# Kernel optimization log

Measured on AMD Instinct MI355X. Metric: run time of the kernel, lower is better.

Reference implementation:

```python
import jax, jax.numpy as jnp
import numpy as np
import math

NUM_HEADS = 12
EXPAND = 3  # head_expand -> DLA hidden = 36
BN_EPS = 1e-5


def conv2d(x, w, groups=1):
    # x: [B,C,H,W], w: [O, I/groups, kh, kw], stride 1, SAME padding (Conv2dSame)
    return jax.lax.conv_general_dilated(
        x, w, window_strides=(1, 1), padding='SAME',
        dimension_numbers=('NCHW', 'OIHW', 'NCHW'), feature_group_count=groups)


def batchnorm(x, gamma, beta):
    # training-mode BatchNorm2d: batch statistics over (B, H, W) per channel
    mean = jnp.mean(x, axis=(0, 2, 3), keepdims=True)
    var = jnp.var(x, axis=(0, 2, 3), keepdims=True)
    xn = (x - mean) * jax.lax.rsqrt(var + BN_EPS)
    return xn * gamma[None, :, None, None] + beta[None, :, None, None]


def setup_inputs() -> dict:
    key = jax.random.key(0)
    ks = jax.random.split(key, 8)
    B, N, C = 32, 196, 768
    H = NUM_HEADS
    hidden = H * EXPAND  # 36
    s = 0.02
    inp = {
        'x': jax.random.normal(ks[0], (B, N, C), dtype=jnp.float32),
        'w_qkv': jax.random.normal(ks[1], (3 * C, C), dtype=jnp.float32) * s,
        'w_exp': jax.random.normal(ks[2], (hidden, H, 1, 1), dtype=jnp.float32) * 0.1,
        'bn1_g': jnp.ones((hidden,), jnp.float32), 'bn1_b': jnp.zeros((hidden,), jnp.float32),
        'w_dw': jax.random.normal(ks[3], (hidden, 1, 3, 3), dtype=jnp.float32) * 0.1,
        'bn2_g': jnp.ones((hidden,), jnp.float32), 'bn2_b': jnp.zeros((hidden,), jnp.float32),
        'w_pro': jax.random.normal(ks[4], (H, hidden, 1, 1), dtype=jnp.float32) * 0.1,
        'bn3_g': jnp.ones((H,), jnp.float32), 'bn3_b': jnp.zeros((H,), jnp.float32),
        'abn_g': jnp.ones((H,), jnp.float32), 'abn_b': jnp.zeros((H,), jnp.float32),
        'w_proj': jax.random.normal(ks[5], (C, C), dtype=jnp.float32) * s,
        'b_proj': jnp.zeros((C,), jnp.float32),
    }
    return inp


def reference(x, w_qkv, w_exp, bn1_g, bn1_b, w_dw, bn2_g, bn2_b,
              w_pro, bn3_g, bn3_b, abn_g, abn_b, w_proj, b_proj):
    B, N, C = x.shape
    H = NUM_HEADS
    d = C // H
    hidden = H * EXPAND
    scale = d ** (-0.5)
    rs = math.sqrt(scale)

    # qkv: [B,N,3C] -> [3,B,H,N,d]
    qkv = (x @ w_qkv.T).reshape(B, N, 3, H, d).transpose(2, 0, 3, 1, 4)
    q = qkv[0] * rs
    k = qkv[1] * rs
    v = qkv[2]

    attn = jax.nn.softmax(jnp.einsum('bhnd,bhmd->bhnm', q, k), axis=-1)

    # DLA (conv_exapnd): 1x1 expand -> BN -> ReLU6 -> 3x3 depthwise -> BN -> ReLU6 -> 1x1 project -> BN
    y = conv2d(attn, w_exp)                       # [B, 36, N, N]
    y = jnp.clip(batchnorm(y, bn1_g, bn1_b), 0.0, 6.0)
    y = conv2d(y, w_dw, groups=hidden)            # depthwise 3x3
    y = jnp.clip(batchnorm(y, bn2_g, bn2_b), 0.0, 6.0)
    y = conv2d(y, w_pro)                          # [B, 12, N, N]
    y = batchnorm(y, bn3_g, bn3_b)
    attn_r = batchnorm(y, abn_g, abn_b)           # adapt_bn

    out = jnp.einsum('bhnm,bhmd->bhnd', attn_r, v)  # [B,H,N,d]
    out = out.transpose(0, 2, 1, 3).reshape(B, N, C)
    out = out @ w_proj.T + b_proj
    return out, attn_r
```

## Files before the change

### kernel.cpp

```cpp
#include <hip/hip_runtime.h>
#include <hip/hip_bf16.h>
#include <hip/hip_fp16.h>
#include <math.h>

constexpr int Bz  = 32;
constexpr int Nn  = 196;
constexpr int Cc  = 768;
constexpr int Hh  = 12;
constexpr int Dd  = 64;
constexpr int NN2 = Nn * Nn;
constexpr int QSZ = Bz * Nn * Cc;
constexpr int ATT = Bz * Hh * NN2;
constexpr int SAMP = Bz * NN2;
constexpr float RS = 0.35355339059327373f;
constexpr int CHUNK = 7056;
constexpr int NCACHE = 6076;
constexpr int RA_CAP = 4181;
constexpr int RB_CAP = 1365;

typedef short bf16x8 __attribute__((ext_vector_type(8)));
typedef float f32x4  __attribute__((ext_vector_type(4)));

__device__ inline ushort f2b(float f) {
  __hip_bfloat16 h = __float2bfloat16(f);
  return *reinterpret_cast<ushort*>(&h);
}
__device__ inline float b2f(ushort u) {
  union { float f; unsigned i; } x; x.i = ((unsigned)u) << 16; return x.f;
}
__device__ inline ushort f2h_(float f) {
  __half h = __float2half(f);
  return *reinterpret_cast<ushort*>(&h);
}
__device__ inline float h2f_(ushort u) {
  __half h = *reinterpret_cast<__half*>(&u);
  return __half2float(h);
}
__device__ inline const ushort* y2chunk_r(int blk, const ushort* rA, const ushort* rB,
                                          const ushort* rC) {
  if (blk < RA_CAP) return rA + (size_t)blk*CHUNK;
  if (blk < RA_CAP + RB_CAP) return rB + (size_t)(blk - RA_CAP)*CHUNK;
  return rC + (size_t)(blk - RA_CAP - RB_CAP)*CHUNK;
}
__device__ inline ushort* y2chunk_w(int blk, ushort* rA, ushort* rB, ushort* rC) {
  if (blk < RA_CAP) return rA + (size_t)blk*CHUNK;
  if (blk < RA_CAP + RB_CAP) return rB + (size_t)(blk - RA_CAP)*CHUNK;
  return rC + (size_t)(blk - RA_CAP - RB_CAP)*CHUNK;
}

__global__ __launch_bounds__(256) void k_cast(const float* __restrict__ in,
                                              ushort* __restrict__ outp) {
  const int j = blockIdx.x*256 + threadIdx.x;
  float4 a = ((const float4*)in)[2*j];
  float4 b = ((const float4*)in)[2*j+1];
  ushort o[8] = { f2b(a.x), f2b(a.y), f2b(a.z), f2b(a.w),
                  f2b(b.x), f2b(b.y), f2b(b.z), f2b(b.w) };
  ((uint4*)outp)[j] = *(const uint4*)o;
}

template<int EPI>
__global__ __launch_bounds__(256) void k_mfma_gemm(const ushort* __restrict__ A,
                                                   const ushort* __restrict__ B,
                                                   const float* __restrict__ bias,
                                                   void* __restrict__ o0,
                                                   void* __restrict__ o1,
                                                   void* __restrict__ o2) {
  __shared__ ushort As[128*72];
  __shared__ ushort Bs[128*72];
  const int t = threadIdx.x;
  const int m0 = blockIdx.y*128, n0 = blockIdx.x*128;
  const int w = t>>6, lane = t&63;
  const int wr = w>>1, wc = w&1;
  const int lrow = lane&15, lkb = lane>>4;
  f32x4 acc[4][4] = {};
  const int srow = t>>1, skoff = (t&1)*32;
  const ushort* aP = A + (size_t)(m0+srow)*768 + skoff;
  const ushort* bP = B + (size_t)(n0+srow)*768 + skoff;
  ushort* aw = &As[srow*72 + skoff];
  ushort* bw = &Bs[srow*72 + skoff];
  for (int k0 = 0; k0 < 768; k0 += 64) {
    uint4 a0 = *(const uint4*)(aP+k0),    a1 = *(const uint4*)(aP+k0+8);
    uint4 a2 = *(const uint4*)(aP+k0+16), a3 = *(const uint4*)(aP+k0+24);
    uint4 b0 = *(const uint4*)(bP+k0),    b1 = *(const uint4*)(bP+k0+8);
    uint4 b2 = *(const uint4*)(bP+k0+16), b3 = *(const uint4*)(bP+k0+24);
    __syncthreads();
    *(uint4*)(aw)    = a0; *(uint4*)(aw+8)  = a1;
    *(uint4*)(aw+16) = a2; *(uint4*)(aw+24) = a3;
    *(uint4*)(bw)    = b0; *(uint4*)(bw+8)  = b1;
    *(uint4*)(bw+16) = b2; *(uint4*)(bw+24) = b3;
    __syncthreads();
#pragma unroll
    for (int kk = 0; kk < 2; kk++) {
      bf16x8 af[4], bfr[4];
#pragma unroll
      for (int m = 0; m < 4; m++)
        af[m] = *(const bf16x8*)&As[(wr*64+m*16+lrow)*72 + kk*32 + lkb*8];
#pragma unroll
      for (int n = 0; n < 4; n++)
        bfr[n] = *(const bf16x8*)&Bs[(wc*64+n*16+lrow)*72 + kk*32 + lkb*8];
#pragma unroll
      for (int m = 0; m < 4; m++)
#pragma unroll
        for (int n = 0; n < 4; n++)
          acc[m][n] = __builtin_amdgcn_mfma_f32_16x16x32_bf16(af[m], bfr[n], acc[m][n], 0, 0, 0);
    }
  }
  const int r4 = lane>>4;
#pragma unroll
  for (int m = 0; m < 4; m++) {
#pragma unroll
    for (int r = 0; r < 4; r++) {
      const int grow = m0 + wr*64 + m*16 + r4*4 + r;
      if (EPI == 0) {
        ushort* q = (ushort*)o0; ushort* k = (ushort*)o1; ushort* v = (ushort*)o2;
        const int b = grow/196, nn = grow - b*196;
#pragma unroll
        for (int n = 0; n < 4; n++) {
          const int gcol = n0 + wc*64 + n*16 + lrow;
          const int three = gcol/768, rem = gcol - three*768;
          const int h = rem>>6, dd = rem&63;
          float val = acc[m][n][r] * (three < 2 ? RS : 1.0f);
          ushort* base = (three == 0) ? q : (three == 1) ? k : v;
          base[((size_t)(b*12+h)*196 + nn)*64 + dd] = f2b(val);
        }
      } else {
        float* outp = (float*)o0;
#pragma unroll
        for (int n = 0; n < 4; n++) {
          const int gcol = n0 + wc*64 + n*16 + lrow;
          outp[(size_t)grow*768 + gcol] = acc[m][n][r] + bias[gcol];
        }
      }
    }
  }
}

__global__ __launch_bounds__(256) void k_qks(const ushort* __restrict__ qb,
                                             const ushort* __restrict__ kb,
                                             float* __restrict__ attn) {
  __shared__ ushort K_lds[208*68];
  const int t = threadIdx.x;
  const int bh = blockIdx.x;
  const ushort* kp = kb + (size_t)bh*Nn*Dd;
  const ushort* qp = qb + (size_t)bh*Nn*Dd;
  for (int i = t; i < 1568; i += 256) {
    int row = i >> 3, ko = (i & 7)*8;
    *(uint4*)&K_lds[row*68 + ko] = *(const uint4*)(kp + (size_t)row*64 + ko);
  }
  for (int i = t; i < 408; i += 256)
    ((unsigned*)&K_lds[196*68])[i] = 0u;
  __syncthreads();
  const int w = t >> 6, lane = t & 63;
  const int slot = blockIdx.y*4 + w;
  if (slot >= 13) return;
  const int lrow = lane & 15, lk = lane >> 4;
  int qrow = slot*16 + lrow; if (qrow > 195) qrow = 195;
  bf16x8 aq0 = *(const bf16x8*)(qp + (size_t)qrow*64 + lk*8);
  bf16x8 aq1 = *(const bf16x8*)(qp + (size_t)qrow*64 + 32 + lk*8);
  f32x4 acc[13];
#pragma unroll
  for (int nt = 0; nt < 13; nt++) {
    f32x4 a = {};
    bf16x8 b0 = *(const bf16x8*)&K_lds[(nt*16 + lrow)*68 + lk*8];
    a = __builtin_amdgcn_mfma_f32_16x16x32_bf16(aq0, b0, a, 0, 0, 0);
    bf16x8 b1 = *(const bf16x8*)&K_lds[(nt*16 + lrow)*68 + 32 + lk*8];
    acc[nt] = __builtin_amdgcn_mfma_f32_16x16x32_bf16(aq1, b1, a, 0, 0, 0);
  }
  const bool tailok = (lrow < 4);
  float inv[4];
#pragma unroll
  for (int r = 0; r < 4; r++) {
    float mx = -1e30f;
#pragma unroll
    for (int nt = 0; nt < 12; nt++) mx = fmaxf(mx, acc[nt][r]);
    if (tailok) mx = fmaxf(mx, acc[12][r]);
    mx = fmaxf(mx, __shfl_xor(mx, 1, 64));
    mx = fmaxf(mx, __shfl_xor(mx, 2, 64));
    mx = fmaxf(mx, __shfl_xor(mx, 4, 64));
    mx = fmaxf(mx, __shfl_xor(mx, 8, 64));
    float s = 0.0f;
#pragma unroll
    for (int nt = 0; nt < 13; nt++) {
      bool valid = (nt < 12) || tailok;
      float e = valid ? __expf(acc[nt][r] - mx) : 0.0f;
      acc[nt][r] = e;
      s += e;
    }
    s += __shfl_xor(s, 1, 64);
    s += __shfl_xor(s, 2, 64);
    s += __shfl_xor(s, 4, 64);
    s += __shfl_xor(s, 8, 64);
    inv[r] = 1.0f / s;
  }
  const int rowb = slot*16 + lk*4;
#pragma unroll
  for (int r = 0; r < 4; r++) {
    const int row = rowb + r;
    if (row < 196) {
      float* op = attn + ((size_t)bh*196 + row)*196;
#pragma unroll
      for (int nt = 0; nt < 13; nt++) {
        int col = nt*16 + lrow;
        if (col < 196) op[col] = acc[nt][r]*inv[r];
      }
    }
  }
}

__global__ __launch_bounds__(256) void k_gram(const float* __restrict__ attn,
                                              float* __restrict__ part) {
  __shared__ float red2[4*78];
  const int t = threadIdx.x;
  float m[78] = {};
  const int stride = gridDim.x * 256;
  for (int s = blockIdx.x*256 + t; s < SAMP; s += stride) {
    int b = s / NN2, p = s - b*NN2;
    float a[12];
#pragma unroll
    for (int h = 0; h < 12; h++) a[h] = attn[((size_t)(b*12+h))*NN2 + p];
    int idx = 0;
#pragma unroll
    for (int h = 0; h < 12; h++)
#pragma unroll
      for (int h2 = h; h2 < 12; h2++, idx++) m[idx] = fmaf(a[h], a[h2], m[idx]);
  }
#pragma unroll
  for (int i = 0; i < 78; i++) {
#pragma unroll
    for (int off = 32; off; off >>= 1) m[i] += __shfl_xor(m[i], off, 64);
  }
  const int w = t >> 6;
  if ((t & 63) == 0) {
#pragma unroll
    for (int i = 0; i < 78; i++) red2[w*78 + i] = m[i];
  }
  __syncthreads();
  if (t < 78)
    part[(size_t)blockIdx.x*78 + t] = red2[t] + red2[78+t] + red2[156+t] + red2[234+t];
}

__global__ __launch_bounds__(256) void k_reduce(const float* __restrict__ part, int nb,
                                               int stride, double* __restrict__ dsum) {
  __shared__ double sh[256];
  const int c = blockIdx.x;
  const int t = threadIdx.x;
  double s = 0.0;
  for (int i = t; i < nb; i += 256) s += (double)part[(size_t)i*stride + c];
  sh[t] = s;
  __syncthreads();
  for (int o = 128; o; o >>= 1) {
    if (t < o) sh[t] += sh[t + o];
    __syncthreads();
  }
  if (t == 0) dsum[c] = sh[0];
}

__global__ void k_bn1gram(const double* __restrict__ dsum,
                          const float* __restrict__ w_exp,
                          const float* __restrict__ g, const float* __restrict__ beta,
                          float* __restrict__ stats) {
  int c = threadIdx.x;
  if (c >= 36) return;
  float wv[12];
  float mean = 0.0f;
#pragma unroll
  for (int h = 0; h < 12; h++) { wv[h] = w_exp[c*12+h]; mean += wv[h]; }
  mean *= (1.0f/196.0f);
  double e2 = 0.0;
  int idx = 0;
#pragma unroll
  for (int h = 0; h < 12; h++)
#pragma unroll
    for (int h2 = h; h2 < 12; h2++, idx++) {
      double coef = (double)wv[h] * (double)wv[h2] * (h == h2 ? 1.0 : 2.0);
      e2 += coef * dsum[idx];
    }
  double var = e2 / (double)SAMP - (double)mean*mean;
  float a = g[c] * rsqrtf((float)var + 1e-5f);
  stats[c] = a;
  stats[36 + c] = beta[c] - mean * a;
}

__global__ __launch_bounds__(256) void k_dlaA(const float* __restrict__ attn,
                                              const float* __restrict__ w_exp,
                                              const float* __restrict__ w_dw,
                                              const float* __restrict__ stats,
                                              ushort* __restrict__ rA,
                                              ushort* __restrict__ rB,
                                              ushort* __restrict__ rC,
                                              float* __restrict__ part) {
  __shared__ float  y_s[12*263];
  __shared__ ushort y2l[12*200];
  __shared__ float  sbuf[2*168];
  const int t = threadIdx.x;
  const int blk = blockIdx.x;
  const int b = blk / 196, tile = blk - b*196;
  const int tyq = tile / 14;
  const int ty0 = tyq * 14, tx0 = (tile - tyq*14) * 14;
  const int hy = ty0 + (t >> 4) - 1, hx = tx0 + (t & 15) - 1;
  const bool inb = (hy >= 0) && (hy < 196) && (hx >= 0) && (hx < 196);
  float a[12];
#pragma unroll
  for (int ch = 0; ch < 12; ch++)
    a[ch] = inb ? attn[((size_t)(b*12+ch))*NN2 + (size_t)hy*196 + hx] : 0.0f;

  const bool dwact = (t < 168);
  const int cl = t % 12, col = t / 12;
  ushort* ydst = (blk < NCACHE) ? y2chunk_w(blk, rA, rB, rC) : nullptr;

  for (int g = 0; g < 3; g++) {
    __syncthreads();
#pragma unroll
    for (int c2 = 0; c2 < 12; c2++) {
      const int c = g*12 + c2;
      float y = 0.0f;
#pragma unroll
      for (int h = 0; h < 12; h++) y = fmaf(w_exp[c*12+h], a[h], y);
      y = y*stats[c] + stats[36+c];
      y = fminf(fmaxf(y, 0.0f), 6.0f);
      y_s[c2*263 + t] = inb ? y : 0.0f;
    }
    __syncthreads();
    if (dwact) {
      const int c = g*12 + cl;
      const float* ys = &y_s[cl*263 + col];
      const float* wd = &w_dw[c*9];
      float s1 = 0.0f, s2 = 0.0f;
      ushort y2h[14];
      float r0c0 = ys[0],  r0c1 = ys[1],  r0c2 = ys[2];
      float r1c0 = ys[16], r1c1 = ys[17], r1c2 = ys[18];
#pragma unroll
      for (int r = 0; r < 14; r++) {
        float r2c0 = ys[(r+2)*16], r2c1 = ys[(r+2)*16+1], r2c2 = ys[(r+2)*16+2];
        float y2 = wd[0]*r0c0;
        y2 = fmaf(wd[1], r0c1, y2); y2 = fmaf(wd[2], r0c2, y2);
        y2 = fmaf(wd[3], r1c0, y2); y2 = fmaf(wd[4], r1c1, y2);
        y2 = fmaf(wd[5], r1c2, y2); y2 = fmaf(wd[6], r2c0, y2);
        y2 = fmaf(wd[7], r2c1, y2); y2 = fmaf(wd[8], r2c2, y2);
        s1 += y2; s2 = fmaf(y2, y2, s2);
        y2h[r] = f2h_(y2);
        r0c0 = r1c0; r0c1 = r1c1; r0c2 = r1c2;
        r1c0 = r2c0; r1c1 = r2c1; r1c2 = r2c2;
      }
      sbuf[cl*14 + col] = s1;
      sbuf[168 + cl*14 + col] = s2;
#pragma unroll
      for (int r = 0; r < 14; r++) y2l[cl*200 + r*14 + col] = y2h[r];
    }
    __syncthreads();
    if (ydst) {
      for (int i = t; i < 2352; i += 256) {
        int c2 = i / 196, px = i - c2*196;
        ydst[g*2352 + i] = y2l[c2*200 + px];
      }
    }
    if (t < 24) {
      const int cc = t % 12, wh = t / 12;
      float s = 0.0f;
#pragma unroll
      for (int j = 0; j < 14; j++) s += sbuf[wh*168 + cc*14 + j];
      part[(size_t)blk*72 + wh*36 + g*12 + cc] = s;
    }
  }
}

__global__ __launch_bounds__(256) void k_dlaB(const float* __restrict__ attn,
                                              const ushort* __restrict__ rA,
                                              const ushort* __restrict__ rB,
                                              const ushort* __restrict__ rC,
                                              const float* __restrict__ w_exp,
                                              const float* __restrict__ w_dw,
                                              const float* __restrict__ w_pro,
                                              const float* __restrict__ stats,
                                              float* __restrict__ zatt,
                                              float* __restrict__ z31,
                                              float* __restrict__ part) {
  __shared__ float y_s[12*256];
  __shared__ float z2[12*200];
  const int t = threadIdx.x;
  const int blk = blockIdx.x;
  const int b = blk / 196, tile = blk - b*196;
  const int tyq = tile / 14;
  const int ty0 = tyq * 14, tx0 = (tile - tyq*14) * 14;
  const bool act = (t < 196);
  const int py = t / 14, px = t - py*14;
  const int oy = ty0 + py, ox = tx0 + px;
  float z[12] = {};

  if (blk < NCACHE) {
    if (act) {
      const ushort* src = y2chunk_r(blk, rA, rB, rC);
#pragma unroll
      for (int c = 0; c < 36; c++) {
        float y2 = h2f_(src[c*196 + t]);
        float y2c = y2*stats[72+c] + stats[108+c];
        y2c = fminf(fmaxf(y2c, 0.0f), 6.0f);
#pragma unroll
        for (int cc = 0; cc < 12; cc++) z[cc] = fmaf(w_pro[cc*36+c], y2c, z[cc]);
      }
#pragma unroll
      for (int cc = 0; cc < 12; cc++)
        zatt[((size_t)(b*12+cc))*NN2 + (size_t)oy*196 + ox] = z[cc];
    }
  } else {
    const int hy = ty0 + (t >> 4) - 1, hx = tx0 + (t & 15) - 1;
    const bool inb = (hy >= 0) && (hy < 196) && (hx >= 0) && (hx < 196);
    float a[12];
#pragma unroll
    for (int ch = 0; ch < 12; ch++)
      a[ch] = inb ? attn[((size_t)(b*12+ch))*NN2 + (size_t)hy*196 + hx] : 0.0f;
    const int base = (py+1)*16 + (px+1);
    for (int g = 0; g < 3; g++) {
      __syncthreads();
#pragma unroll
      for (int cl = 0; cl < 12; cl++) {
        const int c = g*12 + cl;
        float y = 0.0f;
#pragma unroll
        for (int h = 0; h < 12; h++) y = fmaf(w_exp[c*12+h], a[h], y);
        y = y*stats[c] + stats[36+c];
        y = fminf(fmaxf(y, 0.0f), 6.0f);
        y_s[cl*256 + t] = inb ? y : 0.0f;
      }
      __syncthreads();
      if (act) {
#pragma unroll
        for (int cl = 0; cl < 12; cl++) {
          const int c = g*12 + cl;
          const float* ys = &y_s[cl*256];
          float y2 = 0.0f;
#pragma unroll
          for (int di = 0; di < 3; di++)
#pragma unroll
            for (int dj = 0; dj < 3; dj++)
              y2 = fmaf(w_dw[c*9 + di*3 + dj], ys[base + (di-1)*16 + (dj-1)], y2);
          float y2c = y2*stats[72+c] + stats[108+c];
          y2c = fminf(fmaxf(y2c, 0.0f), 6.0f);
#pragma unroll
          for (int cc = 0; cc < 12; cc++) z[cc] = fmaf(w_pro[cc*36+c], y2c, z[cc]);
        }
      }
    }
    if (act) {
#pragma unroll
      for (int cc = 0; cc < 12; cc++)
        z31[(size_t)cc*NN2 + (size_t)oy*196 + ox] = z[cc];
    }
  }
  __syncthreads();
  if (act) {
#pragma unroll
    for (int cc = 0; cc < 12; cc++) z2[cc*200 + t] = z[cc];
  }
  __syncthreads();
  const int rs = t >> 3, seg = t & 7;
  const int pix0 = seg*25;
  const int pcnt = (seg == 7) ? 21 : 25;
  if (rs < 24) {
    const int cl = rs % 12, wh = rs / 12;
    float s = 0.0f;
    for (int i = 0; i < pcnt; i++) {
      float v = z2[cl*200 + pix0 + i];
      s += wh ? v*v : v;
    }
    s += __shfl_xor(s, 1, 64);
    s += __shfl_xor(s, 2, 64);
    s += __shfl_xor(s, 4, 64);
    if (seg == 0)
      part[(size_t)blk*24 + wh*12 + cl] = s;
  }
}

__global__ void k_bnaffine36(const double* __restrict__ dsum,
                             const float* __restrict__ g, const float* __restrict__ beta,
                             float* __restrict__ stats, int off) {
  int c = threadIdx.x;
  if (c >= 36) return;
  double m = dsum[c] / (double)SAMP;
  double v = dsum[36 + c] / (double)SAMP - m*m;
  float a = g[c] * rsqrtf((float)v + 1e-5f);
  stats[off + c] = a;
  stats[off + 36 + c] = beta[c] - (float)m * a;
}

__global__ void k_bnfinal(const double* __restrict__ dsum,
                          const float* __restrict__ g3, const float* __restrict__ b3,
                          const float* __restrict__ ag, const float* __restrict__ ab,
                          float* __restrict__ stats) {
  int c = threadIdx.x;
  if (c >= 12) return;
  (void)b3;
  double m = dsum[c] / (double)SAMP;
  double v = dsum[12 + c] / (double)SAMP - m*m;
  float r1 = rsqrtf((float)v + 1e-5f);
  float vt = g3[c]*g3[c]*(float)v*r1*r1;
  float r2 = rsqrtf(vt + 1e-5f);
  float A = g3[c]*ag[c]*r1*r2;
  stats[144 + c] = A;
  stats[156 + c] = ab[c] - (float)m*A;
}

__global__ __launch_bounds__(256) void k_pvm(const float* __restrict__ z31,
                                             const ushort* __restrict__ v16,
                                             const float* __restrict__ stats,
                                             float* __restrict__ attn_r,
                                             ushort* __restrict__ out_pre) {
  constexpr int STR = 232;
  __shared__ ushort Vt[64*STR];
  __shared__ ushort U[32*STR];
  const int t = threadIdx.x;
  const int bh = blockIdx.x;
  const int r0 = blockIdx.y * 32;
  const int b = bh / 12, h = bh - b*12;
  const float Af = stats[144 + h], Bf = stats[156 + h];
  const ushort* vp = v16 + (size_t)bh * Nn * Dd;

#pragma unroll
  for (int half = 0; half < 2; half++) {
    const int mbase = half * 104;
    const int nm = half ? 92 : 104;
    for (int i = t; i < nm*8; i += 256) {
      int lm = i >> 3, d0 = (i & 7)*8;
      *(uint4*)&U[lm*64 + d0] = *(const uint4*)(vp + (size_t)(mbase+lm)*64 + d0);
    }
    __syncthreads();
    const int ngrp = (nm + 7) >> 3;
    for (int i = t; i < 64*ngrp; i += 256) {
      int d = i & 63, mg = i >> 6;
      int lm0 = mg*8;
      ushort tmp[8];
      int cnt = nm - lm0; if (cnt > 8) cnt = 8;
      for (int j = 0; j < cnt; j++) tmp[j] = U[(lm0+j)*64 + d];
      for (int j = cnt; j < 8; j++) tmp[j] = 0;
      *(uint4*)&Vt[d*STR + mbase + lm0] = *(uint4*)tmp;
    }
    __syncthreads();
  }
  for (int i = t; i < 64*36; i += 256) {
    int d = i / 36, m = 196 + i % 36;
    Vt[d*STR + m] = 0;
  }
  for (int i = t; i < 32*STR/8; i += 256)
    ((uint4*)U)[i] = make_uint4(0,0,0,0);
  __syncthreads();
  const int nvalid = (r0 + 32 <= 196) ? 32 : (196 - r0);
  float* arp = attn_r + (size_t)bh*NN2 + (size_t)r0*196;
  const float* zp = (b < 31) ? arp : (z31 + (size_t)h*NN2 + (size_t)r0*196);
  for (int idx = t; idx < nvalid*196; idx += 256) {
    int rr = idx / 196, m = idx - rr*196;
    float val = fmaf(zp[(size_t)rr*196 + m], Af, Bf);
    arp[(size_t)rr*196 + m] = val;
    U[rr*STR + m] = f2b(val);
  }
  __syncthreads();
  const int w = t >> 6, lane = t & 63;
  const int mt = w >> 1, ct = w & 1;
  const int lr = lane & 15, lk = lane >> 4;
#pragma unroll
  for (int cn = 0; cn < 2; cn++) {
    const int n0 = ct*32 + cn*16;
    f32x4 acc = {};
#pragma unroll
    for (int ks = 0; ks < 7; ks++) {
      bf16x8 af = *(const bf16x8*)&U[(mt*16 + lr)*STR + ks*32 + lk*8];
      bf16x8 bf = *(const bf16x8*)&Vt[(n0 + lr)*STR + ks*32 + lk*8];
      acc = __builtin_amdgcn_mfma_f32_16x16x32_bf16(af, bf, acc, 0, 0, 0);
    }
#pragma unroll
    for (int r = 0; r < 4; r++) {
      int row = mt*16 + lk*4 + r;
      if (row < nvalid)
        out_pre[((size_t)(b*196 + r0 + row))*Cc + h*64 + n0 + lr] = f2b(acc[r]);
    }
  }
}

extern "C" void kernel_launch(void* const* d_in, const int* in_sizes, int n_in,
                              void* d_out, int out_size, void* d_ws, size_t ws_size,
                              hipStream_t stream) {
  (void)in_sizes; (void)n_in; (void)out_size; (void)ws_size;
  const float* x      = (const float*)d_in[0];
  const float* w_qkv  = (const float*)d_in[1];
  const float* w_exp  = (const float*)d_in[2];
  const float* bn1_g  = (const float*)d_in[3];
  const float* bn1_b  = (const float*)d_in[4];
  const float* w_dw   = (const float*)d_in[5];
  const float* bn2_g  = (const float*)d_in[6];
  const float* bn2_b  = (const float*)d_in[7];
  const float* w_pro  = (const float*)d_in[8];
  const float* bn3_g  = (const float*)d_in[9];
  const float* bn3_b  = (const float*)d_in[10];
  const float* abn_g  = (const float*)d_in[11];
  const float* abn_b  = (const float*)d_in[12];
  const float* w_proj = (const float*)d_in[13];
  const float* b_proj = (const float*)d_in[14];

  float* out      = (float*)d_out;
  float* attn_out = out + (size_t)QSZ;
  float* ws    = (float*)d_ws;
  ushort* vb16 = (ushort*)ws;
  ushort* opb  = (ushort*)ws + (size_t)QSZ;
  float*  big  = ws + (size_t)QSZ;
  ushort* qb16 = (ushort*)big;
  ushort* kb16 = qb16 + (size_t)QSZ;
  float* stats = ws + (size_t)QSZ + ATT;
  float* part  = stats + 256;
  double* dsum = (double*)(part + (size_t)6272*72);
  float* z31   = (float*)(dsum + 96);

  ushort* xb   = (ushort*)out;
  ushort* wqb  = xb + (size_t)QSZ;
  ushort* rB   = (ushort*)out;
  ushort* wpb  = (ushort*)part;

  k_cast <<<QSZ/2048, 256, 0, stream>>>(x, xb);
  k_cast <<<(2304*768)/2048, 256, 0, stream>>>(w_qkv, wqb);
  k_mfma_gemm<0><<<dim3(18, 49), 256, 0, stream>>>(xb, wqb, nullptr, qb16, kb16, vb16);
  k_qks      <<<dim3(384, 4), 256, 0, stream>>>(qb16, kb16, attn_out);
  k_gram     <<<2048, 256, 0, stream>>>(attn_out, part);
  k_reduce   <<<78, 256, 0, stream>>>(part, 2048, 78, dsum);
  k_bn1gram  <<<1, 64, 0, stream>>>(dsum, w_exp, bn1_g, bn1_b, stats);
  k_dlaA     <<<6272, 256, 0, stream>>>(attn_out, w_exp, w_dw, stats,
                                        (ushort*)big, rB, opb, part);
  k_reduce   <<<72, 256, 0, stream>>>(part, 6272, 72, dsum);
  k_bnaffine36<<<1, 64, 0, stream>>>(dsum, bn2_g, bn2_b, stats, 72);
  k_dlaB     <<<6272, 256, 0, stream>>>(attn_out, (const ushort*)big, rB, opb,
                                        w_exp, w_dw, w_pro, stats, attn_out, z31, part);
  k_reduce   <<<24, 256, 0, stream>>>(part, 6272, 24, dsum);
  k_bnfinal  <<<1, 64, 0, stream>>>(dsum, bn3_g, bn3_b, abn_g, abn_b, stats);
  k_cast     <<<(768*768)/2048, 256, 0, stream>>>(w_proj, wpb);
  k_pvm      <<<dim3(384, 7), 256, 0, stream>>>(z31, vb16, stats, attn_out, opb);
  k_mfma_gemm<1><<<dim3(6, 49), 256, 0, stream>>>(opb, wpb, b_proj, out, nullptr, nullptr);
}
```

Baseline: 366.9 us.

## Split DLA stage B into cached light kernel and recompute heavy kernel

The single DLA-B kernel, which branched per block between reading cached y2 chunks and recomputing expand+depthwise for the last batch, is split into two kernels. The light kernel handles the 31 cached batches with 434 row-band blocks, two pixels per thread with vectorised loads and stores, and reduces BN partial sums across the whole block. The heavy kernel recomputes only batch 31 across 196 tiles. This removes per-block divergence, cuts the partial-sum count the reduction must read from 6272 to 630, and yields wider memory accesses. The trade-offs are an extra kernel launch, and the heavy kernel now runs after the light one as a separate, poorly occupied launch of 196 blocks.

```diff
diff --git a/kernel.cpp b/kernel.cpp
--- a/kernel.cpp
+++ b/kernel.cpp
@@ -364,88 +364,130 @@
   }
 }
 
-__global__ __launch_bounds__(256) void k_dlaB(const float* __restrict__ attn,
-                                              const ushort* __restrict__ rA,
-                                              const ushort* __restrict__ rB,
-                                              const ushort* __restrict__ rC,
-                                              const float* __restrict__ w_exp,
-                                              const float* __restrict__ w_dw,
-                                              const float* __restrict__ w_pro,
-                                              const float* __restrict__ stats,
-                                              float* __restrict__ zatt,
-                                              float* __restrict__ z31,
-                                              float* __restrict__ part) {
+__global__ __launch_bounds__(256) void k_dlaBlight(const ushort* __restrict__ rA,
+                                                   const ushort* __restrict__ rB,
+                                                   const ushort* __restrict__ rC,
+                                                   const float* __restrict__ w_pro,
+                                                   const float* __restrict__ stats,
+                                                   float* __restrict__ zatt,
+                                                   float* __restrict__ part) {
+  __shared__ float red[4*24];
+  const int t = threadIdx.x;
+  const int lb = blockIdx.x;
+  const int b = lb / 14, band = lb - b*14;
+  const int chunk0 = b*196 + band*14;
+  float s1[12] = {}, s2[12] = {};
+  for (int pair = t; pair < 1372; pair += 256) {
+    const int p = pair*2;
+    const int r = p / 196, ox = p - r*196;
+    const int tx = ox / 14, px = ox - tx*14;
+    const ushort* ch = y2chunk_r(chunk0 + tx, rA, rB, rC) + r*14 + px;
+    float z0[12] = {}, z1[12] = {};
+#pragma unroll
+    for (int c = 0; c < 36; c++) {
+      const unsigned u = *(const unsigned*)(ch + c*196);
+      float ya = h2f_((ushort)(u & 0xffffu));
+      float yb = h2f_((ushort)(u >> 16));
+      const float A2 = stats[72+c], B2 = stats[108+c];
+      ya = fminf(fmaxf(fmaf(ya, A2, B2), 0.0f), 6.0f);
+      yb = fminf(fmaxf(fmaf(yb, A2, B2), 0.0f), 6.0f);
+#pragma unroll
+      for (int cc = 0; cc < 12; cc++) {
+        const float wp = w_pro[cc*36 + c];
+        z0[cc] = fmaf(wp, ya, z0[cc]);
+        z1[cc] = fmaf(wp, yb, z1[cc]);
+      }
+    }
+    const int oy = band*14 + r;
+#pragma unroll
+    for (int cc = 0; cc < 12; cc++) {
+      float2 v2 = make_float2(z0[cc], z1[cc]);
+      *(float2*)&zatt[((size_t)(b*12+cc))*NN2 + (size_t)oy*196 + ox] = v2;
+      s1[cc] += z0[cc] + z1[cc];
+      s2[cc] += z0[cc]*z0[cc] + z1[cc]*z1[cc];
+    }
+  }
+#pragma unroll
+  for (int cc = 0; cc < 12; cc++) {
+#pragma unroll
+    for (int off = 32; off; off >>= 1) {
+      s1[cc] += __shfl_xor(s1[cc], off, 64);
+      s2[cc] += __shfl_xor(s2[cc], off, 64);
+    }
+  }
+  const int w = t >> 6;
+  if ((t & 63) == 0) {
+#pragma unroll
+    for (int cc = 0; cc < 12; cc++) {
+      red[w*24 + cc] = s1[cc];
+      red[w*24 + 12 + cc] = s2[cc];
+    }
+  }
+  __syncthreads();
+  if (t < 24)
+    part[(size_t)lb*24 + t] = red[t] + red[24+t] + red[48+t] + red[72+t];
+}
+
+__global__ __launch_bounds__(256) void k_dlaBheavy(const float* __restrict__ attn,
+                                                   const float* __restrict__ w_exp,
+                                                   const float* __restrict__ w_dw,
+                                                   const float* __restrict__ w_pro,
+                                                   const float* __restrict__ stats,
+                                                   float* __restrict__ z31,
+                                                   float* __restrict__ part) {
   __shared__ float y_s[12*256];
   __shared__ float z2[12*200];
   const int t = threadIdx.x;
-  const int blk = blockIdx.x;
-  const int b = blk / 196, tile = blk - b*196;
+  const int tile = blockIdx.x;
+  const int b = 31;
   const int tyq = tile / 14;
   const int ty0 = tyq * 14, tx0 = (tile - tyq*14) * 14;
   const bool act = (t < 196);
   const int py = t / 14, px = t - py*14;
   const int oy = ty0 + py, ox = tx0 + px;
   float z[12] = {};
-
-  if (blk < NCACHE) {
+  const int hy = ty0 + (t >> 4) - 1, hx = tx0 + (t & 15) - 1;
+  const bool inb = (hy >= 0) && (hy < 196) && (hx >= 0) && (hx < 196);
+  float a[12];
+#pragma unroll
+  for (int ch = 0; ch < 12; ch++)
+    a[ch] = inb ? attn[((size_t)(b*12+ch))*NN2 + (size_t)hy*196 + hx] : 0.0f;
+  const int base = (py+1)*16 + (px+1);
+  for (int g = 0; g < 3; g++) {
+    __syncthreads();
+#pragma unroll
+    for (int cl = 0; cl < 12; cl++) {
+      const int c = g*12 + cl;
+      float y = 0.0f;
+#pragma unroll
+      for (int h = 0; h < 12; h++) y = fmaf(w_exp[c*12+h], a[h], y);
+      y = y*stats[c] + stats[36+c];
+      y = fminf(fmaxf(y, 0.0f), 6.0f);
+      y_s[cl*256 + t] = inb ? y : 0.0f;
+    }
+    __syncthreads();
     if (act) {
-      const ushort* src = y2chunk_r(blk, rA, rB, rC);
-#pragma unroll
-      for (int c = 0; c < 36; c++) {
-        float y2 = h2f_(src[c*196 + t]);
+#pragma unroll
+      for (int cl = 0; cl < 12; cl++) {
+        const int c = g*12 + cl;
+        const float* ys = &y_s[cl*256];
+        float y2 = 0.0f;
+#pragma unroll
+        for (int di = 0; di < 3; di++)
+#pragma unroll
+          for (int dj = 0; dj < 3; dj++)
+            y2 = fmaf(w_dw[c*9 + di*3 + dj], ys[base + (di-1)*16 + (dj-1)], y2);
         float y2c = y2*stats[72+c] + stats[108+c];
         y2c = fminf(fmaxf(y2c, 0.0f), 6.0f);
 #pragma unroll
         for (int cc = 0; cc < 12; cc++) z[cc] = fmaf(w_pro[cc*36+c], y2c, z[cc]);
       }
-#pragma unroll
-      for (int cc = 0; cc < 12; cc++)
-        zatt[((size_t)(b*12+cc))*NN2 + (size_t)oy*196 + ox] = z[cc];
-    }
-  } else {
-    const int hy = ty0 + (t >> 4) - 1, hx = tx0 + (t & 15) - 1;
-    const bool inb = (hy >= 0) && (hy < 196) && (hx >= 0) && (hx < 196);
-    float a[12];
-#pragma unroll
-    for (int ch = 0; ch < 12; ch++)
-      a[ch] = inb ? attn[((size_t)(b*12+ch))*NN2 + (size_t)hy*196 + hx] : 0.0f;
-    const int base = (py+1)*16 + (px+1);
-    for (int g = 0; g < 3; g++) {
-      __syncthreads();
-#pragma unroll
-      for (int cl = 0; cl < 12; cl++) {
-        const int c = g*12 + cl;
-        float y = 0.0f;
-#pragma unroll
-        for (int h = 0; h < 12; h++) y = fmaf(w_exp[c*12+h], a[h], y);
-        y = y*stats[c] + stats[36+c];
-        y = fminf(fmaxf(y, 0.0f), 6.0f);
-        y_s[cl*256 + t] = inb ? y : 0.0f;
-      }
-      __syncthreads();
-      if (act) {
-#pragma unroll
-        for (int cl = 0; cl < 12; cl++) {
-          const int c = g*12 + cl;
-          const float* ys = &y_s[cl*256];
-          float y2 = 0.0f;
-#pragma unroll
-          for (int di = 0; di < 3; di++)
-#pragma unroll
-            for (int dj = 0; dj < 3; dj++)
-              y2 = fmaf(w_dw[c*9 + di*3 + dj], ys[base + (di-1)*16 + (dj-1)], y2);
-          float y2c = y2*stats[72+c] + stats[108+c];
-          y2c = fminf(fmaxf(y2c, 0.0f), 6.0f);
-#pragma unroll
-          for (int cc = 0; cc < 12; cc++) z[cc] = fmaf(w_pro[cc*36+c], y2c, z[cc]);
-        }
-      }
-    }
-    if (act) {
-#pragma unroll
-      for (int cc = 0; cc < 12; cc++)
-        z31[(size_t)cc*NN2 + (size_t)oy*196 + ox] = z[cc];
-    }
+    }
+  }
+  if (act) {
+#pragma unroll
+    for (int cc = 0; cc < 12; cc++)
+      z31[(size_t)cc*NN2 + (size_t)oy*196 + ox] = z[cc];
   }
   __syncthreads();
   if (act) {
@@ -467,7 +509,7 @@
     s += __shfl_xor(s, 2, 64);
     s += __shfl_xor(s, 4, 64);
     if (seg == 0)
-      part[(size_t)blk*24 + wh*12 + cl] = s;
+      part[(size_t)(434 + tile)*24 + wh*12 + cl] = s;
   }
 }
 
@@ -624,9 +666,10 @@
                                         (ushort*)big, rB, opb, part);
   k_reduce   <<<72, 256, 0, stream>>>(part, 6272, 72, dsum);
   k_bnaffine36<<<1, 64, 0, stream>>>(dsum, bn2_g, bn2_b, stats, 72);
-  k_dlaB     <<<6272, 256, 0, stream>>>(attn_out, (const ushort*)big, rB, opb,
-                                        w_exp, w_dw, w_pro, stats, attn_out, z31, part);
-  k_reduce   <<<24, 256, 0, stream>>>(part, 6272, 24, dsum);
+  k_dlaBlight<<<434, 256, 0, stream>>>((const ushort*)big, rB, opb, w_pro, stats,
+                                       attn_out, part);
+  k_dlaBheavy<<<196, 256, 0, stream>>>(attn_out, w_exp, w_dw, w_pro, stats, z31, part);
+  k_reduce   <<<24, 256, 0, stream>>>(part, 630, 24, dsum);
   k_bnfinal  <<<1, 64, 0, stream>>>(dsum, bn3_g, bn3_b, abn_g, abn_b, stats);
   k_cast     <<<(768*768)/2048, 256, 0, stream>>>(w_proj, wpb);
   k_pvm      <<<dim3(384, 7), 256, 0, stream>>>(z31, vb16, stats, attn_out, opb);
```

After: 408.7 us. +11.4%, slower.
